# Kernel optimization log

Measured on AMD Instinct MI355X. Metric: run time of the kernel, lower is better.

The kernel has to match this reference:

```python
import jax, jax.numpy as jnp
import numpy as np

NEG_BIG = -9e15  # matches torch's -9000000000000000.0 mask value


def _l2norm(x, eps=1e-12):
    # F.normalize(x, p=2, dim=1)
    n = jnp.sqrt(jnp.sum(x * x, axis=1, keepdims=True))
    return x / jnp.maximum(n, eps)


def _fusion_attribute(emb, att_emb, adj):
    # cosine similarity [N, M]
    sim = _l2norm(emb) @ _l2norm(att_emb).T
    sim = sim * adj
    # masked softmax over dim=1: zeros -> -9e15
    logits = jnp.where(sim != 0, sim, jnp.full_like(sim, NEG_BIG))
    attention = jax.nn.softmax(logits, axis=1)
    return attention @ att_emb


def setup_inputs() -> dict:
    key = jax.random.key(0)
    k1, k2, k3, k4 = jax.random.split(key, 4)
    U, I, D = 10000, 8000, 64
    users_emb = 0.1 * jax.random.normal(k1, (U, D), dtype=jnp.float32)  # init.normal_(std=0.1)
    items_emb = 0.1 * jax.random.normal(k2, (I, D), dtype=jnp.float32)
    Out_UserAttNets = (jax.random.uniform(k3, (U, I)) < 0.05).astype(jnp.float32)
    Out_ItemAttNets = (jax.random.uniform(k4, (I, U)) < 0.05).astype(jnp.float32)
    return {
        "num_users": U,
        "num_items": I,
        "users_emb": users_emb,
        "items_emb": items_emb,
        "Out_UserAttNets": Out_UserAttNets,
        "Out_ItemAttNets": Out_ItemAttNets,
    }


def reference(num_users, num_items, users_emb, items_emb, Out_UserAttNets, Out_ItemAttNets):
    out_useratt_emb = _fusion_attribute(users_emb, items_emb, Out_UserAttNets)
    out_itematt_emb = _fusion_attribute(items_emb, users_emb, Out_ItemAttNets)
    return (users_emb, items_emb, out_useratt_emb, out_itematt_emb)
```

## Files before the change

kernel.cpp:

```cpp
#include <hip/hip_runtime.h>
#include <math.h>

typedef float f32x4 __attribute__((ext_vector_type(4)));
typedef unsigned int u32;
typedef u32 u32x4 __attribute__((ext_vector_type(4)));
typedef unsigned short u16;
typedef unsigned long long u64;

#define SEGCAP 768

__device__ __forceinline__ u16 f2b(float x) {
    union { float f; u32 u; } v; v.f = x;
    return (u16)((v.u + 0x7FFFu + ((v.u >> 16) & 1u)) >> 16);
}
__device__ __forceinline__ float b2f_lo(u32 u) { union { u32 u; float f; } v; v.u = u << 16;         return v.f; }
__device__ __forceinline__ float b2f_hi(u32 u) { union { u32 u; float f; } v; v.u = u & 0xFFFF0000u; return v.f; }

__global__ __launch_bounds__(256) void prep_kernel(
    const float* __restrict__ users, const float* __restrict__ items,
    u16* __restrict__ hU, u16* __restrict__ hI,
    float* __restrict__ nU, float* __restrict__ nI, int U, int I)
{
    int lane = threadIdx.x & 63;
    int row  = (blockIdx.x << 2) + (threadIdx.x >> 6);
    const float* src; u16* hat; float* nrm; int r;
    if (row < U) { r = row; src = users; hat = hU; nrm = nU; }
    else { r = row - U; if (r >= I) return; src = items; hat = hI; nrm = nI; }
    float x = src[(size_t)r * 64 + lane];
    float s = x * x;
#pragma unroll
    for (int off = 32; off; off >>= 1) s += __shfl_xor(s, off, 64);
    float nv   = sqrtf(s);
    float rinv = 1.0f / fmaxf(nv, 1e-12f);
    hat[(size_t)r * 64 + lane] = f2b(x * rinv);
    if (lane == 0) nrm[r] = nv;
}

__global__ __launch_bounds__(256) void att_row_kernel(
    const float* __restrict__ users, const float* __restrict__ items,
    const u16* __restrict__ hU, const u16* __restrict__ hI,
    const float* __restrict__ nU, const float* __restrict__ nI,
    const float* __restrict__ adjU, const float* __restrict__ adjI,
    float* __restrict__ outU, float* __restrict__ outI, int U, int I)
{
    __shared__ int cols_sh[4][SEGCAP];

    const int lane = threadIdx.x & 63;
    const int wid  = threadIdx.x >> 6;
    const int grow = ((int)blockIdx.x << 2) + wid;
    if (grow >= U + I) return;

    const u16* qhat; const u16* kvhat; const float* kvnrm;
    const float* kvraw; const float* adj; float* outp;
    int M, row;
    if (grow < U) {
        row = grow;     qhat = hU; kvhat = hI; kvnrm = nI;
        kvraw = items;  adj = adjU; outp = outU; M = I;
    } else {
        row = grow - U; qhat = hI; kvhat = hU; kvnrm = nU;
        kvraw = users;  adj = adjI; outp = outI; M = U;
    }
    const float* adjrow = adj + (size_t)row * M;

    int wcount = 0;
    const int M4 = M >> 2;
    for (int i4 = lane; i4 < M4; i4 += 64) {
        f32x4 a = __builtin_nontemporal_load((const f32x4*)adjrow + i4);
#pragma unroll
        for (int j = 0; j < 4; ++j) {
            bool pred = (a[j] != 0.0f);
            u64 mask = __ballot(pred);
            if (pred) {
                int pos = wcount + __builtin_amdgcn_mbcnt_hi(
                    (u32)(mask >> 32), __builtin_amdgcn_mbcnt_lo((u32)mask, 0));
                if (pos < SEGCAP) cols_sh[wid][pos] = (i4 << 2) + j;
            }
            wcount += __popcll(mask);
        }
    }
    wcount = __shfl(wcount, 0, 64);
    if (M & 3) {
        int idx = (M4 << 2) + lane;
        bool pred = (idx < M) && (adjrow[idx] != 0.0f);
        u64 mask = __ballot(pred);
        if (pred) {
            int pos = wcount + __builtin_amdgcn_mbcnt_hi(
                (u32)(mask >> 32), __builtin_amdgcn_mbcnt_lo((u32)mask, 0));
            if (pos < SEGCAP) cols_sh[wid][pos] = idx;
        }
        wcount += __popcll(mask);
    }
    int cnt = wcount > SEGCAP ? SEGCAP : wcount;

    const int sub = lane & 7;
    const int grp = lane >> 3;

    u32x4 qw = *(const u32x4*)(qhat + (size_t)row * 64 + sub * 8);
    const float q0 = b2f_lo(qw[0]), q1 = b2f_hi(qw[0]);
    const float q2 = b2f_lo(qw[1]), q3 = b2f_hi(qw[1]);
    const float q4 = b2f_lo(qw[2]), q5 = b2f_hi(qw[2]);
    const float q6 = b2f_lo(qw[3]), q7 = b2f_hi(qw[3]);

    float a0 = 0.f, a1 = 0.f, a2 = 0.f, a3 = 0.f;
    float a4 = 0.f, a5 = 0.f, a6 = 0.f, a7 = 0.f, wsum = 0.f;
    const int* cp = cols_sh[wid];

    int i = grp;
    for (; i + 24 < cnt; i += 32) {
        int ca = cp[i], cb = cp[i + 8], cc = cp[i + 16], cd = cp[i + 24];
        u32x4 va = *(const u32x4*)(kvhat + (size_t)ca * 64 + sub * 8);
        u32x4 vb = *(const u32x4*)(kvhat + (size_t)cb * 64 + sub * 8);
        u32x4 vc = *(const u32x4*)(kvhat + (size_t)cc * 64 + sub * 8);
        u32x4 vd = *(const u32x4*)(kvhat + (size_t)cd * 64 + sub * 8);
        float na = kvnrm[ca], nb = kvnrm[cb], nc = kvnrm[cc], nd = kvnrm[cd];
        float ra0 = b2f_lo(va[0]), ra1 = b2f_hi(va[0]), ra2 = b2f_lo(va[1]), ra3 = b2f_hi(va[1]);
        float ra4 = b2f_lo(va[2]), ra5 = b2f_hi(va[2]), ra6 = b2f_lo(va[3]), ra7 = b2f_hi(va[3]);
        float rb0 = b2f_lo(vb[0]), rb1 = b2f_hi(vb[0]), rb2 = b2f_lo(vb[1]), rb3 = b2f_hi(vb[1]);
        float rb4 = b2f_lo(vb[2]), rb5 = b2f_hi(vb[2]), rb6 = b2f_lo(vb[3]), rb7 = b2f_hi(vb[3]);
        float rc0 = b2f_lo(vc[0]), rc1 = b2f_hi(vc[0]), rc2 = b2f_lo(vc[1]), rc3 = b2f_hi(vc[1]);
        float rc4 = b2f_lo(vc[2]), rc5 = b2f_hi(vc[2]), rc6 = b2f_lo(vc[3]), rc7 = b2f_hi(vc[3]);
        float rd0 = b2f_lo(vd[0]), rd1 = b2f_hi(vd[0]), rd2 = b2f_lo(vd[1]), rd3 = b2f_hi(vd[1]);
        float rd4 = b2f_lo(vd[2]), rd5 = b2f_hi(vd[2]), rd6 = b2f_lo(vd[3]), rd7 = b2f_hi(vd[3]);
        float da = fmaf(q0, ra0, fmaf(q1, ra1, fmaf(q2, ra2, fmaf(q3, ra3,
                   fmaf(q4, ra4, fmaf(q5, ra5, fmaf(q6, ra6, q7 * ra7)))))));
        float db = fmaf(q0, rb0, fmaf(q1, rb1, fmaf(q2, rb2, fmaf(q3, rb3,
                   fmaf(q4, rb4, fmaf(q5, rb5, fmaf(q6, rb6, q7 * rb7)))))));
        float dc = fmaf(q0, rc0, fmaf(q1, rc1, fmaf(q2, rc2, fmaf(q3, rc3,
                   fmaf(q4, rc4, fmaf(q5, rc5, fmaf(q6, rc6, q7 * rc7)))))));
        float dd = fmaf(q0, rd0, fmaf(q1, rd1, fmaf(q2, rd2, fmaf(q3, rd3,
                   fmaf(q4, rd4, fmaf(q5, rd5, fmaf(q6, rd6, q7 * rd7)))))));
#pragma unroll
        for (int off = 1; off <= 4; off <<= 1) {
            da += __shfl_xor(da, off, 64);
            db += __shfl_xor(db, off, 64);
            dc += __shfl_xor(dc, off, 64);
            dd += __shfl_xor(dd, off, 64);
        }
        float wa = (da != 0.0f) ? __expf(da - 1.0f) : 0.0f;
        float wb = (db != 0.0f) ? __expf(db - 1.0f) : 0.0f;
        float wc = (dc != 0.0f) ? __expf(dc - 1.0f) : 0.0f;
        float wd = (dd != 0.0f) ? __expf(dd - 1.0f) : 0.0f;
        float xa = wa * na, xb = wb * nb, xc = wc * nc, xd = wd * nd;
        a0 = fmaf(xa, ra0, fmaf(xb, rb0, fmaf(xc, rc0, fmaf(xd, rd0, a0))));
        a1 = fmaf(xa, ra1, fmaf(xb, rb1, fmaf(xc, rc1, fmaf(xd, rd1, a1))));
        a2 = fmaf(xa, ra2, fmaf(xb, rb2, fmaf(xc, rc2, fmaf(xd, rd2, a2))));
        a3 = fmaf(xa, ra3, fmaf(xb, rb3, fmaf(xc, rc3, fmaf(xd, rd3, a3))));
        a4 = fmaf(xa, ra4, fmaf(xb, rb4, fmaf(xc, rc4, fmaf(xd, rd4, a4))));
        a5 = fmaf(xa, ra5, fmaf(xb, rb5, fmaf(xc, rc5, fmaf(xd, rd5, a5))));
        a6 = fmaf(xa, ra6, fmaf(xb, rb6, fmaf(xc, rc6, fmaf(xd, rd6, a6))));
        a7 = fmaf(xa, ra7, fmaf(xb, rb7, fmaf(xc, rc7, fmaf(xd, rd7, a7))));
        if (sub == 0) wsum += (wa + wb) + (wc + wd);
    }
    for (; i < cnt; i += 8) {
        int ca = cp[i];
        u32x4 va = *(const u32x4*)(kvhat + (size_t)ca * 64 + sub * 8);
        float na = kvnrm[ca];
        float ra0 = b2f_lo(va[0]), ra1 = b2f_hi(va[0]), ra2 = b2f_lo(va[1]), ra3 = b2f_hi(va[1]);
        float ra4 = b2f_lo(va[2]), ra5 = b2f_hi(va[2]), ra6 = b2f_lo(va[3]), ra7 = b2f_hi(va[3]);
        float da = fmaf(q0, ra0, fmaf(q1, ra1, fmaf(q2, ra2, fmaf(q3, ra3,
                   fmaf(q4, ra4, fmaf(q5, ra5, fmaf(q6, ra6, q7 * ra7)))))));
#pragma unroll
        for (int off = 1; off <= 4; off <<= 1) da += __shfl_xor(da, off, 64);
        float wa = (da != 0.0f) ? __expf(da - 1.0f) : 0.0f;
        float xa = wa * na;
        a0 = fmaf(xa, ra0, a0); a1 = fmaf(xa, ra1, a1);
        a2 = fmaf(xa, ra2, a2); a3 = fmaf(xa, ra3, a3);
        a4 = fmaf(xa, ra4, a4); a5 = fmaf(xa, ra5, a5);
        a6 = fmaf(xa, ra6, a6); a7 = fmaf(xa, ra7, a7);
        if (sub == 0) wsum += wa;
    }

#pragma unroll
    for (int off = 8; off <= 32; off <<= 1) {
        wsum += __shfl_xor(wsum, off, 64);
        a0 += __shfl_xor(a0, off, 64); a1 += __shfl_xor(a1, off, 64);
        a2 += __shfl_xor(a2, off, 64); a3 += __shfl_xor(a3, off, 64);
        a4 += __shfl_xor(a4, off, 64); a5 += __shfl_xor(a5, off, 64);
        a6 += __shfl_xor(a6, off, 64); a7 += __shfl_xor(a7, off, 64);
    }
    float den = __shfl(wsum, 0, 64);

    if (lane < 8) {
        float* orow = outp + (size_t)row * 64 + lane * 8;
        if (den > 0.0f) {
            float inv = 1.0f / den;
            ((f32x4*)orow)[0] = (f32x4){a0 * inv, a1 * inv, a2 * inv, a3 * inv};
            ((f32x4*)orow)[1] = (f32x4){a4 * inv, a5 * inv, a6 * inv, a7 * inv};
        } else {
            f32x4 m0 = (f32x4){0.f, 0.f, 0.f, 0.f};
            f32x4 m1 = (f32x4){0.f, 0.f, 0.f, 0.f};
            for (int r = 0; r < M; ++r) {
                const f32x4* kr = (const f32x4*)(kvraw + (size_t)r * 64 + lane * 8);
                m0 += kr[0]; m1 += kr[1];
            }
            float invM = 1.0f / (float)M;
            ((f32x4*)orow)[0] = m0 * invM;
            ((f32x4*)orow)[1] = m1 * invM;
        }
    }
}

extern "C" void kernel_launch(void* const* d_in, const int* in_sizes, int n_in,
                              void* d_out, int out_size, void* d_ws, size_t ws_size,
                              hipStream_t stream) {
    const float* users = (const float*)d_in[2];
    const float* items = (const float*)d_in[3];
    const float* adjU  = (const float*)d_in[4];
    const float* adjI  = (const float*)d_in[5];
    const int U = in_sizes[2] / 64;
    const int I = in_sizes[3] / 64;

    char* w = (char*)d_ws;
    u16* hU = (u16*)w;    w += (size_t)U * 64 * sizeof(u16);
    u16* hI = (u16*)w;    w += (size_t)I * 64 * sizeof(u16);
    float* nU = (float*)w; w += (size_t)U * sizeof(float);
    float* nI = (float*)w;

    float* out = (float*)d_out;

    hipMemcpyAsync(out, users, (size_t)U * 64 * sizeof(float),
                   hipMemcpyDeviceToDevice, stream);
    hipMemcpyAsync(out + (size_t)U * 64, items, (size_t)I * 64 * sizeof(float),
                   hipMemcpyDeviceToDevice, stream);

    prep_kernel<<<(U + I + 3) / 4, 256, 0, stream>>>(users, items, hU, hI, nU, nI, U, I);

    float* outUatt = out + (size_t)(U + I) * 64;
    float* outIatt = outUatt + (size_t)U * 64;
    att_row_kernel<<<(U + I + 3) / 4, 256, 0, stream>>>(
        users, items, hU, hI, nU, nI, adjU, adjI, outUatt, outIatt, U, I);
}
```

Measured before the change: 237.2 us.

## Split each attention row across two wavefronts and combine through shared memory

Each row is now handled by two wavefronts, each scanning half of the adjacency row and gathering half of the nonzero columns. Partial weighted sums and denominators are combined in shared memory after a block barrier, and the grid doubles. This targets per-row latency in the adjacency scan and the gather phase by spreading each row over more parallel work. In exchange it adds a __syncthreads, an extra shared-memory reduction, and a smaller per-half column buffer.

```diff
diff --git a/kernel.cpp b/kernel.cpp
--- a/kernel.cpp
+++ b/kernel.cpp
@@ -7,7 +7,7 @@
 typedef unsigned short u16;
 typedef unsigned long long u64;
 
-#define SEGCAP 768
+#define SEG 512
 
 __device__ __forceinline__ u16 f2b(float x) {
     union { float f; u32 u; } v; v.f = x;
@@ -43,159 +43,182 @@
     const float* __restrict__ adjU, const float* __restrict__ adjI,
     float* __restrict__ outU, float* __restrict__ outI, int U, int I)
 {
-    __shared__ int cols_sh[4][SEGCAP];
+    __shared__ int   cols_sh[4][SEG];
+    __shared__ float red[4][8][8];
+    __shared__ float wsum_sh[4];
 
     const int lane = threadIdx.x & 63;
     const int wid  = threadIdx.x >> 6;
-    const int grow = ((int)blockIdx.x << 2) + wid;
-    if (grow >= U + I) return;
-
-    const u16* qhat; const u16* kvhat; const float* kvnrm;
-    const float* kvraw; const float* adj; float* outp;
-    int M, row;
-    if (grow < U) {
-        row = grow;     qhat = hU; kvhat = hI; kvnrm = nI;
-        kvraw = items;  adj = adjU; outp = outU; M = I;
-    } else {
-        row = grow - U; qhat = hI; kvhat = hU; kvnrm = nU;
-        kvraw = users;  adj = adjI; outp = outI; M = U;
+    const int half = wid & 1;
+    const int grow = ((int)blockIdx.x << 1) + (wid >> 1);
+    const bool valid = (grow < U + I);
+
+    const u16* qhat = 0; const u16* kvhat = 0; const float* kvnrm = 0;
+    const float* kvraw = 0; const float* adj = 0; float* outp = 0;
+    int M = 0, row = 0;
+    if (valid) {
+        if (grow < U) {
+            row = grow;     qhat = hU; kvhat = hI; kvnrm = nI;
+            kvraw = items;  adj = adjU; outp = outU; M = I;
+        } else {
+            row = grow - U; qhat = hI; kvhat = hU; kvnrm = nU;
+            kvraw = users;  adj = adjI; outp = outI; M = U;
+        }
     }
-    const float* adjrow = adj + (size_t)row * M;
-
-    int wcount = 0;
-    const int M4 = M >> 2;
-    for (int i4 = lane; i4 < M4; i4 += 64) {
-        f32x4 a = __builtin_nontemporal_load((const f32x4*)adjrow + i4);
-#pragma unroll
-        for (int j = 0; j < 4; ++j) {
-            bool pred = (a[j] != 0.0f);
+
+    const int sub = lane & 7;
+    const int grp = lane >> 3;
+
+    float a0 = 0.f, a1 = 0.f, a2 = 0.f, a3 = 0.f;
+    float a4 = 0.f, a5 = 0.f, a6 = 0.f, a7 = 0.f, wsum = 0.f;
+
+    if (valid) {
+        const float* adjrow = adj + (size_t)row * M;
+
+        const int mid = (M >> 1) & ~3;
+        const int lo4 = half ? (mid >> 2) : 0;
+        const int hi4 = half ? (M >> 2) : (mid >> 2);
+        int wcount = 0;
+        for (int i4 = lo4 + lane; i4 < hi4; i4 += 64) {
+            f32x4 a = __builtin_nontemporal_load((const f32x4*)adjrow + i4);
+#pragma unroll
+            for (int j = 0; j < 4; ++j) {
+                bool pred = (a[j] != 0.0f);
+                u64 mask = __ballot(pred);
+                if (pred) {
+                    int pos = wcount + __builtin_amdgcn_mbcnt_hi(
+                        (u32)(mask >> 32), __builtin_amdgcn_mbcnt_lo((u32)mask, 0));
+                    if (pos < SEG) cols_sh[wid][pos] = (i4 << 2) + j;
+                }
+                wcount += __popcll(mask);
+            }
+        }
+        wcount = __shfl(wcount, 0, 64);
+        if (half && (M & 3)) {
+            int idx = (hi4 << 2) + lane;
+            bool pred = (idx < M) && (adjrow[idx] != 0.0f);
             u64 mask = __ballot(pred);
             if (pred) {
                 int pos = wcount + __builtin_amdgcn_mbcnt_hi(
                     (u32)(mask >> 32), __builtin_amdgcn_mbcnt_lo((u32)mask, 0));
-                if (pos < SEGCAP) cols_sh[wid][pos] = (i4 << 2) + j;
+                if (pos < SEG) cols_sh[wid][pos] = idx;
             }
             wcount += __popcll(mask);
         }
+        int cnt = wcount > SEG ? SEG : wcount;
+
+        u32x4 qw = *(const u32x4*)(qhat + (size_t)row * 64 + sub * 8);
+        const float q0 = b2f_lo(qw[0]), q1 = b2f_hi(qw[0]);
+        const float q2 = b2f_lo(qw[1]), q3 = b2f_hi(qw[1]);
+        const float q4 = b2f_lo(qw[2]), q5 = b2f_hi(qw[2]);
+        const float q6 = b2f_lo(qw[3]), q7 = b2f_hi(qw[3]);
+
+        const int* cp = cols_sh[wid];
+        int i = grp;
+        for (; i + 24 < cnt; i += 32) {
+            int ca = cp[i], cb = cp[i + 8], cc = cp[i + 16], cd = cp[i + 24];
+            u32x4 va = *(const u32x4*)(kvhat + (size_t)ca * 64 + sub * 8);
+            u32x4 vb = *(const u32x4*)(kvhat + (size_t)cb * 64 + sub * 8);
+            u32x4 vc = *(const u32x4*)(kvhat + (size_t)cc * 64 + sub * 8);
+            u32x4 vd = *(const u32x4*)(kvhat + (size_t)cd * 64 + sub * 8);
+            float na = kvnrm[ca], nb = kvnrm[cb], nc = kvnrm[cc], nd = kvnrm[cd];
+            float ra0 = b2f_lo(va[0]), ra1 = b2f_hi(va[0]), ra2 = b2f_lo(va[1]), ra3 = b2f_hi(va[1]);
+            float ra4 = b2f_lo(va[2]), ra5 = b2f_hi(va[2]), ra6 = b2f_lo(va[3]), ra7 = b2f_hi(va[3]);
+            float rb0 = b2f_lo(vb[0]), rb1 = b2f_hi(vb[0]), rb2 = b2f_lo(vb[1]), rb3 = b2f_hi(vb[1]);
+            float rb4 = b2f_lo(vb[2]), rb5 = b2f_hi(vb[2]), rb6 = b2f_lo(vb[3]), rb7 = b2f_hi(vb[3]);
+            float rc0 = b2f_lo(vc[0]), rc1 = b2f_hi(vc[0]), rc2 = b2f_lo(vc[1]), rc3 = b2f_hi(vc[1]);
+            float rc4 = b2f_lo(vc[2]), rc5 = b2f_hi(vc[2]), rc6 = b2f_lo(vc[3]), rc7 = b2f_hi(vc[3]);
+            float rd0 = b2f_lo(vd[0]), rd1 = b2f_hi(vd[0]), rd2 = b2f_lo(vd[1]), rd3 = b2f_hi(vd[1]);
+            float rd4 = b2f_lo(vd[2]), rd5 = b2f_hi(vd[2]), rd6 = b2f_lo(vd[3]), rd7 = b2f_hi(vd[3]);
+            float da = fmaf(q0, ra0, fmaf(q1, ra1, fmaf(q2, ra2, fmaf(q3, ra3,
+                       fmaf(q4, ra4, fmaf(q5, ra5, fmaf(q6, ra6, q7 * ra7)))))));
+            float db = fmaf(q0, rb0, fmaf(q1, rb1, fmaf(q2, rb2, fmaf(q3, rb3,
+                       fmaf(q4, rb4, fmaf(q5, rb5, fmaf(q6, rb6, q7 * rb7)))))));
+            float dc = fmaf(q0, rc0, fmaf(q1, rc1, fmaf(q2, rc2, fmaf(q3, rc3,
+                       fmaf(q4, rc4, fmaf(q5, rc5, fmaf(q6, rc6, q7 * rc7)))))));
+            float dd = fmaf(q0, rd0, fmaf(q1, rd1, fmaf(q2, rd2, fmaf(q3, rd3,
+                       fmaf(q4, rd4, fmaf(q5, rd5, fmaf(q6, rd6, q7 * rd7)))))));
+#pragma unroll
+            for (int off = 1; off <= 4; off <<= 1) {
+                da += __shfl_xor(da, off, 64);
+                db += __shfl_xor(db, off, 64);
+                dc += __shfl_xor(dc, off, 64);
+                dd += __shfl_xor(dd, off, 64);
+            }
+            float wa = (da != 0.0f) ? __expf(da - 1.0f) : 0.0f;
+            float wb = (db != 0.0f) ? __expf(db - 1.0f) : 0.0f;
+            float wc = (dc != 0.0f) ? __expf(dc - 1.0f) : 0.0f;
+            float wd = (dd != 0.0f) ? __expf(dd - 1.0f) : 0.0f;
+            float xa = wa * na, xb = wb * nb, xc = wc * nc, xd = wd * nd;
+            a0 = fmaf(xa, ra0, fmaf(xb, rb0, fmaf(xc, rc0, fmaf(xd, rd0, a0))));
+            a1 = fmaf(xa, ra1, fmaf(xb, rb1, fmaf(xc, rc1, fmaf(xd, rd1, a1))));
+            a2 = fmaf(xa, ra2, fmaf(xb, rb2, fmaf(xc, rc2, fmaf(xd, rd2, a2))));
+            a3 = fmaf(xa, ra3, fmaf(xb, rb3, fmaf(xc, rc3, fmaf(xd, rd3, a3))));
+            a4 = fmaf(xa, ra4, fmaf(xb, rb4, fmaf(xc, rc4, fmaf(xd, rd4, a4))));
+            a5 = fmaf(xa, ra5, fmaf(xb, rb5, fmaf(xc, rc5, fmaf(xd, rd5, a5))));
+            a6 = fmaf(xa, ra6, fmaf(xb, rb6, fmaf(xc, rc6, fmaf(xd, rd6, a6))));
+            a7 = fmaf(xa, ra7, fmaf(xb, rb7, fmaf(xc, rc7, fmaf(xd, rd7, a7))));
+            if (sub == 0) wsum += (wa + wb) + (wc + wd);
+        }
+        for (; i < cnt; i += 8) {
+            int ca = cp[i];
+            u32x4 va = *(const u32x4*)(kvhat + (size_t)ca * 64 + sub * 8);
+            float na = kvnrm[ca];
+            float ra0 = b2f_lo(va[0]), ra1 = b2f_hi(va[0]), ra2 = b2f_lo(va[1]), ra3 = b2f_hi(va[1]);
+            float ra4 = b2f_lo(va[2]), ra5 = b2f_hi(va[2]), ra6 = b2f_lo(va[3]), ra7 = b2f_hi(va[3]);
+            float da = fmaf(q0, ra0, fmaf(q1, ra1, fmaf(q2, ra2, fmaf(q3, ra3,
+                       fmaf(q4, ra4, fmaf(q5, ra5, fmaf(q6, ra6, q7 * ra7)))))));
+#pragma unroll
+            for (int off = 1; off <= 4; off <<= 1) da += __shfl_xor(da, off, 64);
+            float wa = (da != 0.0f) ? __expf(da - 1.0f) : 0.0f;
+            float xa = wa * na;
+            a0 = fmaf(xa, ra0, a0); a1 = fmaf(xa, ra1, a1);
+            a2 = fmaf(xa, ra2, a2); a3 = fmaf(xa, ra3, a3);
+            a4 = fmaf(xa, ra4, a4); a5 = fmaf(xa, ra5, a5);
+            a6 = fmaf(xa, ra6, a6); a7 = fmaf(xa, ra7, a7);
+            if (sub == 0) wsum += wa;
+        }
+
+#pragma unroll
+        for (int off = 8; off <= 32; off <<= 1) {
+            wsum += __shfl_xor(wsum, off, 64);
+            a0 += __shfl_xor(a0, off, 64); a1 += __shfl_xor(a1, off, 64);
+            a2 += __shfl_xor(a2, off, 64); a3 += __shfl_xor(a3, off, 64);
+            a4 += __shfl_xor(a4, off, 64); a5 += __shfl_xor(a5, off, 64);
+            a6 += __shfl_xor(a6, off, 64); a7 += __shfl_xor(a7, off, 64);
+        }
+        if (lane < 8) {
+            f32x4* rp = (f32x4*)&red[wid][lane][0];
+            rp[0] = (f32x4){a0, a1, a2, a3};
+            rp[1] = (f32x4){a4, a5, a6, a7};
+        }
+        if (lane == 0) wsum_sh[wid] = wsum;
     }
-    wcount = __shfl(wcount, 0, 64);
-    if (M & 3) {
-        int idx = (M4 << 2) + lane;
-        bool pred = (idx < M) && (adjrow[idx] != 0.0f);
-        u64 mask = __ballot(pred);
-        if (pred) {
-            int pos = wcount + __builtin_amdgcn_mbcnt_hi(
-                (u32)(mask >> 32), __builtin_amdgcn_mbcnt_lo((u32)mask, 0));
-            if (pos < SEGCAP) cols_sh[wid][pos] = idx;
-        }
-        wcount += __popcll(mask);
-    }
-    int cnt = wcount > SEGCAP ? SEGCAP : wcount;
-
-    const int sub = lane & 7;
-    const int grp = lane >> 3;
-
-    u32x4 qw = *(const u32x4*)(qhat + (size_t)row * 64 + sub * 8);
-    const float q0 = b2f_lo(qw[0]), q1 = b2f_hi(qw[0]);
-    const float q2 = b2f_lo(qw[1]), q3 = b2f_hi(qw[1]);
-    const float q4 = b2f_lo(qw[2]), q5 = b2f_hi(qw[2]);
-    const float q6 = b2f_lo(qw[3]), q7 = b2f_hi(qw[3]);
-
-    float a0 = 0.f, a1 = 0.f, a2 = 0.f, a3 = 0.f;
-    float a4 = 0.f, a5 = 0.f, a6 = 0.f, a7 = 0.f, wsum = 0.f;
-    const int* cp = cols_sh[wid];
-
-    int i = grp;
-    for (; i + 24 < cnt; i += 32) {
-        int ca = cp[i], cb = cp[i + 8], cc = cp[i + 16], cd = cp[i + 24];
-        u32x4 va = *(const u32x4*)(kvhat + (size_t)ca * 64 + sub * 8);
-        u32x4 vb = *(const u32x4*)(kvhat + (size_t)cb * 64 + sub * 8);
-        u32x4 vc = *(const u32x4*)(kvhat + (size_t)cc * 64 + sub * 8);
-        u32x4 vd = *(const u32x4*)(kvhat + (size_t)cd * 64 + sub * 8);
-        float na = kvnrm[ca], nb = kvnrm[cb], nc = kvnrm[cc], nd = kvnrm[cd];
-        float ra0 = b2f_lo(va[0]), ra1 = b2f_hi(va[0]), ra2 = b2f_lo(va[1]), ra3 = b2f_hi(va[1]);
-        float ra4 = b2f_lo(va[2]), ra5 = b2f_hi(va[2]), ra6 = b2f_lo(va[3]), ra7 = b2f_hi(va[3]);
-        float rb0 = b2f_lo(vb[0]), rb1 = b2f_hi(vb[0]), rb2 = b2f_lo(vb[1]), rb3 = b2f_hi(vb[1]);
-        float rb4 = b2f_lo(vb[2]), rb5 = b2f_hi(vb[2]), rb6 = b2f_lo(vb[3]), rb7 = b2f_hi(vb[3]);
-        float rc0 = b2f_lo(vc[0]), rc1 = b2f_hi(vc[0]), rc2 = b2f_lo(vc[1]), rc3 = b2f_hi(vc[1]);
-        float rc4 = b2f_lo(vc[2]), rc5 = b2f_hi(vc[2]), rc6 = b2f_lo(vc[3]), rc7 = b2f_hi(vc[3]);
-        float rd0 = b2f_lo(vd[0]), rd1 = b2f_hi(vd[0]), rd2 = b2f_lo(vd[1]), rd3 = b2f_hi(vd[1]);
-        float rd4 = b2f_lo(vd[2]), rd5 = b2f_hi(vd[2]), rd6 = b2f_lo(vd[3]), rd7 = b2f_hi(vd[3]);
-        float da = fmaf(q0, ra0, fmaf(q1, ra1, fmaf(q2, ra2, fmaf(q3, ra3,
-                   fmaf(q4, ra4, fmaf(q5, ra5, fmaf(q6, ra6, q7 * ra7)))))));
-        float db = fmaf(q0, rb0, fmaf(q1, rb1, fmaf(q2, rb2, fmaf(q3, rb3,
-                   fmaf(q4, rb4, fmaf(q5, rb5, fmaf(q6, rb6, q7 * rb7)))))));
-        float dc = fmaf(q0, rc0, fmaf(q1, rc1, fmaf(q2, rc2, fmaf(q3, rc3,
-                   fmaf(q4, rc4, fmaf(q5, rc5, fmaf(q6, rc6, q7 * rc7)))))));
-        float dd = fmaf(q0, rd0, fmaf(q1, rd1, fmaf(q2, rd2, fmaf(q3, rd3,
-                   fmaf(q4, rd4, fmaf(q5, rd5, fmaf(q6, rd6, q7 * rd7)))))));
-#pragma unroll
-        for (int off = 1; off <= 4; off <<= 1) {
-            da += __shfl_xor(da, off, 64);
-            db += __shfl_xor(db, off, 64);
-            dc += __shfl_xor(dc, off, 64);
-            dd += __shfl_xor(dd, off, 64);
-        }
-        float wa = (da != 0.0f) ? __expf(da - 1.0f) : 0.0f;
-        float wb = (db != 0.0f) ? __expf(db - 1.0f) : 0.0f;
-        float wc = (dc != 0.0f) ? __expf(dc - 1.0f) : 0.0f;
-        float wd = (dd != 0.0f) ? __expf(dd - 1.0f) : 0.0f;
-        float xa = wa * na, xb = wb * nb, xc = wc * nc, xd = wd * nd;
-        a0 = fmaf(xa, ra0, fmaf(xb, rb0, fmaf(xc, rc0, fmaf(xd, rd0, a0))));
-        a1 = fmaf(xa, ra1, fmaf(xb, rb1, fmaf(xc, rc1, fmaf(xd, rd1, a1))));
-        a2 = fmaf(xa, ra2, fmaf(xb, rb2, fmaf(xc, rc2, fmaf(xd, rd2, a2))));
-        a3 = fmaf(xa, ra3, fmaf(xb, rb3, fmaf(xc, rc3, fmaf(xd, rd3, a3))));
-        a4 = fmaf(xa, ra4, fmaf(xb, rb4, fmaf(xc, rc4, fmaf(xd, rd4, a4))));
-        a5 = fmaf(xa, ra5, fmaf(xb, rb5, fmaf(xc, rc5, fmaf(xd, rd5, a5))));
-        a6 = fmaf(xa, ra6, fmaf(xb, rb6, fmaf(xc, rc6, fmaf(xd, rd6, a6))));
-        a7 = fmaf(xa, ra7, fmaf(xb, rb7, fmaf(xc, rc7, fmaf(xd, rd7, a7))));
-        if (sub == 0) wsum += (wa + wb) + (wc + wd);
-    }
-    for (; i < cnt; i += 8) {
-        int ca = cp[i];
-        u32x4 va = *(const u32x4*)(kvhat + (size_t)ca * 64 + sub * 8);
-        float na = kvnrm[ca];
-        float ra0 = b2f_lo(va[0]), ra1 = b2f_hi(va[0]), ra2 = b2f_lo(va[1]), ra3 = b2f_hi(va[1]);
-        float ra4 = b2f_lo(va[2]), ra5 = b2f_hi(va[2]), ra6 = b2f_lo(va[3]), ra7 = b2f_hi(va[3]);
-        float da = fmaf(q0, ra0, fmaf(q1, ra1, fmaf(q2, ra2, fmaf(q3, ra3,
-                   fmaf(q4, ra4, fmaf(q5, ra5, fmaf(q6, ra6, q7 * ra7)))))));
-#pragma unroll
-        for (int off = 1; off <= 4; off <<= 1) da += __shfl_xor(da, off, 64);
-        float wa = (da != 0.0f) ? __expf(da - 1.0f) : 0.0f;
-        float xa = wa * na;
-        a0 = fmaf(xa, ra0, a0); a1 = fmaf(xa, ra1, a1);
-        a2 = fmaf(xa, ra2, a2); a3 = fmaf(xa, ra3, a3);
-        a4 = fmaf(xa, ra4, a4); a5 = fmaf(xa, ra5, a5);
-        a6 = fmaf(xa, ra6, a6); a7 = fmaf(xa, ra7, a7);
-        if (sub == 0) wsum += wa;
-    }
-
-#pragma unroll
-    for (int off = 8; off <= 32; off <<= 1) {
-        wsum += __shfl_xor(wsum, off, 64);
-        a0 += __shfl_xor(a0, off, 64); a1 += __shfl_xor(a1, off, 64);
-        a2 += __shfl_xor(a2, off, 64); a3 += __shfl_xor(a3, off, 64);
-        a4 += __shfl_xor(a4, off, 64); a5 += __shfl_xor(a5, off, 64);
-        a6 += __shfl_xor(a6, off, 64); a7 += __shfl_xor(a7, off, 64);
-    }
-    float den = __shfl(wsum, 0, 64);
-
-    if (lane < 8) {
-        float* orow = outp + (size_t)row * 64 + lane * 8;
-        if (den > 0.0f) {
-            float inv = 1.0f / den;
-            ((f32x4*)orow)[0] = (f32x4){a0 * inv, a1 * inv, a2 * inv, a3 * inv};
-            ((f32x4*)orow)[1] = (f32x4){a4 * inv, a5 * inv, a6 * inv, a7 * inv};
-        } else {
-            f32x4 m0 = (f32x4){0.f, 0.f, 0.f, 0.f};
-            f32x4 m1 = (f32x4){0.f, 0.f, 0.f, 0.f};
-            for (int r = 0; r < M; ++r) {
-                const f32x4* kr = (const f32x4*)(kvraw + (size_t)r * 64 + lane * 8);
-                m0 += kr[0]; m1 += kr[1];
-            }
-            float invM = 1.0f / (float)M;
-            ((f32x4*)orow)[0] = m0 * invM;
-            ((f32x4*)orow)[1] = m1 * invM;
+    __syncthreads();
+
+    if (valid && half == 0) {
+        float den = wsum_sh[wid] + wsum_sh[wid + 1];
+        if (lane < 8) {
+            f32x4* r0p = (f32x4*)&red[wid][lane][0];
+            f32x4* r1p = (f32x4*)&red[wid + 1][lane][0];
+            f32x4 s0 = r0p[0] + r1p[0];
+            f32x4 s1 = r0p[1] + r1p[1];
+            float* orow = outp + (size_t)row * 64 + lane * 8;
+            if (den > 0.0f) {
+                float inv = 1.0f / den;
+                ((f32x4*)orow)[0] = s0 * inv;
+                ((f32x4*)orow)[1] = s1 * inv;
+            } else {
+                f32x4 m0 = (f32x4){0.f, 0.f, 0.f, 0.f};
+                f32x4 m1 = (f32x4){0.f, 0.f, 0.f, 0.f};
+                for (int r = 0; r < M; ++r) {
+                    const f32x4* kr = (const f32x4*)(kvraw + (size_t)r * 64 + lane * 8);
+                    m0 += kr[0]; m1 += kr[1];
+                }
+                float invM = 1.0f / (float)M;
+                ((f32x4*)orow)[0] = m0 * invM;
+                ((f32x4*)orow)[1] = m1 * invM;
+            }
         }
     }
 }
@@ -227,6 +250,6 @@
 
     float* outUatt = out + (size_t)(U + I) * 64;
     float* outIatt = outUatt + (size_t)U * 64;
-    att_row_kernel<<<(U + I + 3) / 4, 256, 0, stream>>>(
+    att_row_kernel<<<(U + I + 1) / 2, 256, 0, stream>>>(
         users, items, hU, hI, nU, nI, adjU, adjI, outUatt, outIatt, U, I);
 }
```

Result: no change. 239.9 us (+1.1%).
